# Optimization experiments

Measured on AMD Instinct MI355X. Metric: run time of the kernel, lower is better.

Reference implementation:

```python
import jax, jax.numpy as jnp
import numpy as np

B, S, D = 2, 2048, 1024
H = 16            # attention heads
KVH = 4           # key/value heads
G = H // KVH      # group_size = 4
HD = D // H       # head_dim = 64
ROPE_THETA = 10000.0


def rope(x):
    # x: [B, S, D]; interleaved-pair rotary embedding over full last dim
    d = x.shape[-1]
    inv_freq = 1.0 / (ROPE_THETA ** (jnp.arange(0, d, 2, dtype=jnp.float32) / d))  # [d/2]
    ang = jnp.arange(x.shape[1], dtype=jnp.float32)[:, None] * inv_freq[None, :]   # [S, d/2]
    cos, sin = jnp.cos(ang), jnp.sin(ang)
    x1, x2 = x[..., 0::2], x[..., 1::2]
    r1 = x1 * cos - x2 * sin
    r2 = x1 * sin + x2 * cos
    out = jnp.stack([r1, r2], axis=-1).reshape(x.shape)
    return out


def setup_inputs() -> dict:
    key = jax.random.key(0)
    kx, kq, kk, kv = jax.random.split(key, 4)
    x = jax.random.normal(kx, (B, S, D), dtype=jnp.float32)
    # mark last 256 positions of batch element 1 as padding via NaN
    x = x.at[1, S - 256:, :].set(jnp.nan)
    scale = 1.0 / np.sqrt(D)
    Wq = jax.random.normal(kq, (D, D), dtype=jnp.float32) * scale
    Wk = jax.random.normal(kk, (D, D // G), dtype=jnp.float32) * scale
    Wv = jax.random.normal(kv, (D, D // G), dtype=jnp.float32) * scale
    return {"x": x, "Wq": Wq, "Wk": Wk, "Wv": Wv}


def reference(x, Wq, Wk, Wv):
    pad = jnp.isnan(x)                      # [B,S,D]
    x = jnp.where(pad, 0.0, x)
    key_pad = jnp.any(pad, axis=-1)         # [B,S] True = padded token

    q = x @ Wq                              # [B,S,D]
    k = jnp.repeat(x @ Wk, G, axis=-1)      # grouped KV, repeat_interleave -> [B,S,D]
    v = jnp.repeat(x @ Wv, G, axis=-1)

    q = rope(q)
    k = rope(k)

    def split_heads(t):
        return t.reshape(B, S, H, HD).transpose(0, 2, 1, 3)  # [B,H,S,HD]

    q, k, v = split_heads(q), split_heads(k), split_heads(v)

    scores = jnp.einsum('bhqd,bhkd->bhqk', q, k) / np.sqrt(HD)
    causal = jnp.tril(jnp.ones((S, S), dtype=bool))
    allow = causal[None, None, :, :] & (~key_pad)[:, None, None, :]
    scores = jnp.where(allow, scores, -1e9)
    attn = jax.nn.softmax(scores, axis=-1)
    out = jnp.einsum('bhqk,bhkd->bhqd', attn, v)
    return out.transpose(0, 2, 1, 3).reshape(B, S, D)
```

## Files before the change

### kernel.cpp

```cpp
#include <hip/hip_runtime.h>
#include <hip/hip_bf16.h>
#include <math.h>

typedef unsigned short u16;
typedef unsigned int u32;
typedef __bf16 bf16x8 __attribute__((ext_vector_type(8)));
typedef float fx4 __attribute__((ext_vector_type(4)));

#define MFMA16(a, b, c) __builtin_amdgcn_mfma_f32_16x16x32_bf16(a, b, c, 0, 0, 0)

static constexpr int Bb = 2, Ss = 2048, Dd = 1024, Hh = 16, DKV = 256;
static constexpr int NQKV = 1536;
static constexpr int ROWS = Bb * Ss;
static constexpr float L2T_OVER = 0.0259525632f;
static constexpr float SC2 = 0.18033688f;
static constexpr int PSTR = 76;

__device__ __forceinline__ u16 f2bf(float f) {
    union { float f; u32 i; } v; v.f = f;
    u32 u = v.i;
    return (u16)((u + 0x7FFFu + ((u >> 16) & 1u)) >> 16);
}
__device__ __forceinline__ u16 bfr(float f) {
    return (u16)((__float_as_uint(f) + 0x8000u) >> 16);
}

__device__ __forceinline__ void gl16(const u16* g, u16* l) {
    __builtin_amdgcn_global_load_lds(
        (const __attribute__((address_space(1))) void*)g,
        (__attribute__((address_space(3))) void*)l, 16, 0, 0);
}

template <int CTRL>
__device__ __forceinline__ float dppf(float x) {
    return __int_as_float(
        __builtin_amdgcn_mov_dpp(__float_as_int(x), CTRL, 0xF, 0xF, true));
}
__device__ __forceinline__ float rsum16(float x) {
    x += dppf<0xB1>(x);
    x += dppf<0x4E>(x);
    x += dppf<0x124>(x);
    x += dppf<0x128>(x);
    return x;
}

__global__ void pre_kernel(const float* __restrict__ x, const float* __restrict__ Wq,
                           const float* __restrict__ Wk, const float* __restrict__ Wv,
                           u16* __restrict__ xc, u32* __restrict__ kpb,
                           u16* __restrict__ wAll) {
    __shared__ u16 tile[32][33];
    __shared__ int flag;
    int bid = blockIdx.x, t = threadIdx.x;
    if (bid < 4096) {
        int row = bid;
        if (t == 0) flag = 0;
        __syncthreads();
        float4 d = *(const float4*)(x + (size_t)row * Dd + t * 4);
        int any = 0;
        float a0 = d.x, a1 = d.y, a2 = d.z, a3 = d.w;
        if ((__float_as_uint(a0) & 0x7FFFFFFFu) > 0x7F800000u) { a0 = 0.f; any = 1; }
        if ((__float_as_uint(a1) & 0x7FFFFFFFu) > 0x7F800000u) { a1 = 0.f; any = 1; }
        if ((__float_as_uint(a2) & 0x7FFFFFFFu) > 0x7F800000u) { a2 = 0.f; any = 1; }
        if ((__float_as_uint(a3) & 0x7FFFFFFFu) > 0x7F800000u) { a3 = 0.f; any = 1; }
        if (any) atomicOr(&flag, 1);
        uint2 o;
        o.x = (u32)f2bf(a0) | ((u32)f2bf(a1) << 16);
        o.y = (u32)f2bf(a2) | ((u32)f2bf(a3) << 16);
        *(uint2*)(xc + (size_t)row * Dd + t * 4) = o;
        __syncthreads();
        if (t == 0 && flag) {
            int b = row >> 11, s = row & (Ss - 1);
            atomicOr(&kpb[b * 64 + (s >> 5)], 1u << (s & 31));
        }
        return;
    }
    const float* in; u16* out; int C, bx, by;
    if (bid < 5120) { int i = bid - 4096; in = Wq; out = wAll; C = Dd; bx = i & 31; by = i >> 5; }
    else if (bid < 5376) { int i = bid - 5120; in = Wk; out = wAll + (size_t)Dd * Dd; C = DKV; bx = i & 7; by = i >> 3; }
    else { int i = bid - 5376; in = Wv; out = wAll + (size_t)1280 * Dd; C = DKV; bx = i & 7; by = i >> 3; }
    int c0 = bx * 32, r0 = by * 32;
    int tx = t & 31, ty = t >> 5;
    for (int i = 0; i < 32; i += 8)
        tile[ty + i][tx] = f2bf(in[(size_t)(r0 + ty + i) * C + c0 + tx]);
    __syncthreads();
    for (int i = 0; i < 32; i += 8)
        out[(size_t)(c0 + ty + i) * Dd + r0 + tx] = tile[tx][ty + i];
}

__global__ __launch_bounds__(256) void gemm_qkv(
    const u16* __restrict__ A, const u16* __restrict__ Bt, u16* __restrict__ C) {
    __shared__ __align__(16) u16 As[2][128 * 32];
    __shared__ __align__(16) u16 Bs[2][64 * 32];
    int t = threadIdx.x, w = t >> 6, lane = t & 63;
    int l15 = lane & 15, quad = lane >> 4;
    int col0 = blockIdx.x * 64, row0 = blockIdx.y * 128;
    int wm = w >> 1, wn = w & 1;
    fx4 acc[4][2];
#pragma unroll
    for (int i = 0; i < 4; ++i)
#pragma unroll
        for (int j = 0; j < 2; ++j) acc[i][j] = (fx4){0.f, 0.f, 0.f, 0.f};

    auto stage = [&](int kb, int buf) {
#pragma unroll
        for (int i = 0; i < 2; ++i) {
            int slot = i * 256 + t;
            int row = slot >> 2, p = slot & 3, g = p ^ ((row >> 1) & 3);
            gl16(A + (size_t)(row0 + row) * Dd + kb * 32 + g * 8,
                 &As[buf][(i * 256 + w * 64) * 8]);
        }
        {
            int row = t >> 2, p = t & 3, g = p ^ ((row >> 1) & 3);
            gl16(Bt + (size_t)(col0 + row) * Dd + kb * 32 + g * 8,
                 &Bs[buf][(w * 64) * 8]);
        }
    };

    stage(0, 0);
    int buf = 0;
    for (int kb = 0; kb < 32; ++kb) {
        __syncthreads();
        if (kb + 1 < 32) stage(kb + 1, buf ^ 1);
        bf16x8 af[4], bfr2[2];
#pragma unroll
        for (int mi = 0; mi < 4; ++mi) {
            int row = wm * 64 + mi * 16 + l15;
            af[mi] = *(const bf16x8*)(&As[buf][row * 32 + ((quad ^ ((row >> 1) & 3)) * 8)]);
        }
#pragma unroll
        for (int ni = 0; ni < 2; ++ni) {
            int row = wn * 32 + ni * 16 + l15;
            bfr2[ni] = *(const bf16x8*)(&Bs[buf][row * 32 + ((quad ^ ((row >> 1) & 3)) * 8)]);
        }
#pragma unroll
        for (int mi = 0; mi < 4; ++mi)
#pragma unroll
            for (int ni = 0; ni < 2; ++ni)
                acc[mi][ni] = MFMA16(af[mi], bfr2[ni], acc[mi][ni]);
        buf ^= 1;
    }
#pragma unroll
    for (int mi = 0; mi < 4; ++mi) {
        int rbase = row0 + wm * 64 + mi * 16 + quad * 4;
#pragma unroll
        for (int ni = 0; ni < 2; ++ni) {
            int ccol = col0 + wn * 32 + ni * 16 + l15;
#pragma unroll
            for (int r = 0; r < 4; ++r)
                C[(size_t)(rbase + r) * NQKV + ccol] = f2bf(acc[mi][ni][r]);
        }
    }
}

__global__ void post_kernel(const u16* __restrict__ qkv, u16* __restrict__ kr,
                            u16* __restrict__ vtb) {
    __shared__ u16 tile[32][33];
    int bid = blockIdx.x, t = threadIdx.x;
    if (bid < 4096) {
        int row = bid;
        float pos = (float)(row & (Ss - 1));
        float kv = __uint_as_float(((u32)qkv[(size_t)row * NQKV + Dd + t]) << 16);
        float j0 = (float)(2 * t), j1 = j0 + 1.0f;
        float f0 = exp2f(-j0 * L2T_OVER), f1 = exp2f(-j1 * L2T_OVER);
        float s0, c0, s1, c1;
        sincosf(pos * f0, &s0, &c0);
        sincosf(pos * f1, &s1, &c1);
        float r0 = kv * (c0 - s0), r1 = kv * (s0 + c0);
        float r2 = kv * (c1 - s1), r3 = kv * (s1 + c1);
        uint2 o;
        o.x = (u32)f2bf(r0) | ((u32)f2bf(r1) << 16);
        o.y = (u32)f2bf(r2) | ((u32)f2bf(r3) << 16);
        *(uint2*)(kr + (size_t)row * Dd + t * 4) = o;
        return;
    }
    int i = bid - 4096;
    int b = i >> 9, by = (i & 511) >> 3, bx = i & 7;
    int c0 = bx * 32, r0 = by * 32;
    int tx = t & 31, ty = t >> 5;
    for (int k = 0; k < 32; k += 8)
        tile[ty + k][tx] = qkv[(size_t)(b * Ss + r0 + ty + k) * NQKV + 1280 + c0 + tx];
    __syncthreads();
    for (int k = 0; k < 32; k += 8)
        vtb[(size_t)(b * DKV + c0 + ty + k) * Ss + r0 + tx] = tile[tx][ty + k];
}

__device__ __forceinline__ bf16x8 ropeFrag(uint4 raw, float pos, float jbase) {
    u32 W[4] = {raw.x, raw.y, raw.z, raw.w};
    union { u32 u[4]; bf16x8 v; } o;
#pragma unroll
    for (int c = 0; c < 4; ++c) {
        float x0 = __uint_as_float(W[c] << 16);
        float x1 = __uint_as_float(W[c] & 0xFFFF0000u);
        float f = exp2f(-(jbase + (float)c) * L2T_OVER);
        float sn, cs;
        sincosf(pos * f, &sn, &cs);
        float r0 = x0 * cs - x1 * sn, r1 = x0 * sn + x1 * cs;
        o.u[c] = (u32)f2bf(r0) | ((u32)f2bf(r1) << 16);
    }
    return o.v;
}

__global__ __launch_bounds__(256) void attn_kernel(
    const u16* __restrict__ qkv, const u16* __restrict__ kr,
    const u16* __restrict__ vt, const u32* __restrict__ kpb,
    float* __restrict__ O16, float* __restrict__ Lsum) {
    __shared__ __align__(16) u16 Ks[2][64 * 64];
    __shared__ __align__(16) u16 Ps[4][16 * PSTR];

    int t = threadIdx.x, w = t >> 6, lane = t & 63;
    int l15 = lane & 15, quad = lane >> 4;
    int bid = blockIdx.x;
    int u = bid >> 5;
    int tile, c;
    if (u < 32)      { tile = 24 + (u & 7); c = u >> 3; }
    else if (u < 56) { tile = 16 + ((u - 32) & 7); c = (u - 32) >> 3; }
    else if (u < 72) { tile = 8 + ((u - 56) & 7); c = (u - 56) >> 3; }
    else             { tile = u - 72; c = 0; }
    int hh = bid & 31, b = hh >> 4, h = hh & 15;
    int q0 = tile * 64;
    int kb0 = c * 8;
    int kbe = min(kb0 + 8, tile + 1);

    int pos = q0 + w * 16 + l15;
    const u16* qp = qkv + (size_t)(b * Ss + pos) * NQKV + h * 64;
    float jb = (float)(h * 32 + quad * 4);
    bf16x8 qf0 = ropeFrag(*(const uint4*)(qp + quad * 8), (float)pos, jb);
    bf16x8 qf1 = ropeFrag(*(const uint4*)(qp + 32 + quad * 8), (float)pos, jb + 16.f);

    u32 pw_all = kpb[b * 64 + lane];

    const u16* vrow = vt + (size_t)(b * DKV + h * 16 + l15) * Ss;

    auto stageK = [&](int k0, int buf) {
#pragma unroll
        for (int i2 = 0; i2 < 2; ++i2) {
            int row = i2 * 32 + w * 8 + (lane >> 3);
            int gg = (lane & 7) ^ (row & 7);
            gl16(kr + (size_t)(b * Ss + k0 + row) * Dd + h * 64 + gg * 8,
                 &Ks[buf][(i2 * 32 + w * 8) * 64]);
        }
    };

    float l_lane[4] = {0.f, 0.f, 0.f, 0.f};
    fx4 oacc = (fx4){0.f, 0.f, 0.f, 0.f};

    stageK(kb0 * 64, 0);
    int buf = 0;
    const int qrb = q0 + w * 16 + quad * 4;
    const int qmin = q0 + w * 16;

    for (int kb = kb0; kb < kbe; ++kb) {
        int k0 = kb * 64;
        __syncthreads();
        if (kb + 1 < kbe) stageK(k0 + 64, buf ^ 1);

        bf16x8 vf0 = *(const bf16x8*)(vrow + k0 + quad * 8);
        bf16x8 vf1 = *(const bf16x8*)(vrow + k0 + 32 + quad * 8);

        fx4 s[4];
#pragma unroll
        for (int tt = 0; tt < 4; ++tt) {
            const u16* kb_ = &Ks[buf][(tt * 16 + l15) * 64];
            bf16x8 kf0 = *(const bf16x8*)(kb_ + ((quad ^ (l15 & 7)) * 8));
            bf16x8 kf1 = *(const bf16x8*)(kb_ + (((quad + 4) ^ (l15 & 7)) * 8));
            fx4 z = (fx4){0.f, 0.f, 0.f, 0.f};
            fx4 a = MFMA16(qf0, kf0, z);
            s[tt] = MFMA16(qf1, kf1, a);
        }

        u32 pw0 = (u32)__shfl((int)pw_all, 2 * kb, 64);
        u32 pw1 = (u32)__shfl((int)pw_all, 2 * kb + 1, 64);
        bool fast = (k0 + 63 <= qmin) & ((pw0 | pw1) == 0u);

        float e[4][4];
        if (fast) {
#pragma unroll
            for (int tt = 0; tt < 4; ++tt)
#pragma unroll
                for (int r = 0; r < 4; ++r)
                    e[tt][r] = exp2f(fmaf(s[tt][r], SC2, -32.f));
        } else {
            u32 padb[4];
#pragma unroll
            for (int tt = 0; tt < 4; ++tt)
                padb[tt] = ((tt & 2 ? pw1 : pw0) >> ((tt * 16 + l15) & 31)) & 1u;
#pragma unroll
            for (int r = 0; r < 4; ++r) {
                int qq = qrb + r;
#pragma unroll
                for (int tt = 0; tt < 4; ++tt) {
                    float ee = exp2f(fmaf(s[tt][r], SC2, -32.f));
                    e[tt][r] = (k0 + tt * 16 + l15 <= qq && !padb[tt]) ? ee : 0.f;
                }
            }
        }

#pragma unroll
        for (int r = 0; r < 4; ++r) {
            l_lane[r] += (e[0][r] + e[1][r]) + (e[2][r] + e[3][r]);
            int prow = (quad * 4 + r) * PSTR + l15;
            Ps[w][prow + 0] = bfr(e[0][r]);
            Ps[w][prow + 16] = bfr(e[1][r]);
            Ps[w][prow + 32] = bfr(e[2][r]);
            Ps[w][prow + 48] = bfr(e[3][r]);
        }

        {
            bf16x8 pf0 = *(const bf16x8*)(&Ps[w][l15 * PSTR + quad * 8]);
            bf16x8 pf1 = *(const bf16x8*)(&Ps[w][l15 * PSTR + 32 + quad * 8]);
            oacc = MFMA16(pf0, vf0, oacc);
            oacc = MFMA16(pf1, vf1, oacc);
        }
        buf ^= 1;
    }

    size_t obase = (size_t)hh * Ss;
#pragma unroll
    for (int r = 0; r < 4; ++r) {
        float l_row = rsum16(l_lane[r]);
        int q = qrb + r;
        atomicAdd(&O16[(obase + q) * 16 + l15], oacc[r]);
        if (l15 == 0) atomicAdd(&Lsum[obase + q], l_row);
    }
}

__global__ void norm_kernel(const float* __restrict__ O16, const float* __restrict__ Lsum,
                            float* __restrict__ out) {
    int idx = blockIdx.x * 256 + threadIdx.x;
    int d4 = idx & 255;
    int row = idx >> 8;
    int h = d4 >> 4, f = d4 & 15;
    int b = row >> 11, s = row & (Ss - 1);
    size_t o = (size_t)(b * 16 + h) * Ss + s;
    float a = O16[o * 16 + f] / Lsum[o];
    float4 o4 = {a, a, a, a};
    *(float4*)(out + (size_t)row * Dd + d4 * 4) = o4;
}

extern "C" void kernel_launch(void* const* d_in, const int* in_sizes, int n_in,
                              void* d_out, int out_size, void* d_ws, size_t ws_size,
                              hipStream_t stream) {
    const float* x = (const float*)d_in[0];
    const float* Wq = (const float*)d_in[1];
    const float* Wk = (const float*)d_in[2];
    const float* Wv = (const float*)d_in[3];
    float* out = (float*)d_out;

    char* ws = (char*)d_ws;
    const size_t SZ_XC = (size_t)ROWS * Dd * 2;
    const size_t SZ_KPB = 4096;
    const size_t SZ_WALL = (size_t)NQKV * Dd * 2;
    const size_t SZ_QKV = (size_t)ROWS * NQKV * 2;
    const size_t SZ_O16 = (size_t)32 * Ss * 16 * 4;
    const size_t SZ_L = (size_t)32 * Ss * 4;

    size_t off = 0;
    u16* xc = (u16*)(ws + off);
    u16* krope = (u16*)(ws + off); off += SZ_XC;
    u32* kpb = (u32*)(ws + off); off += SZ_KPB;
    u16* wAll = (u16*)(ws + off);
    u16* vtb = (u16*)(ws + off); off += SZ_WALL;
    u16* qkv = (u16*)(ws + off); off += SZ_QKV;
    float* O16 = (float*)(ws + off); off += SZ_O16;
    float* Ls = (float*)(ws + off); off += SZ_L;
    (void)ws_size; (void)in_sizes; (void)n_in; (void)out_size;

    hipMemsetAsync(kpb, 0, 2 * 64 * 4, stream);
    hipMemsetAsync(O16, 0, SZ_O16 + SZ_L, stream);
    pre_kernel<<<5632, 256, 0, stream>>>(x, Wq, Wk, Wv, xc, kpb, wAll);
    gemm_qkv<<<dim3(NQKV / 64, ROWS / 128), 256, 0, stream>>>(xc, wAll, qkv);
    post_kernel<<<5120, 256, 0, stream>>>(qkv, krope, vtb);
    attn_kernel<<<2560, 256, 0, stream>>>(qkv, krope, vtb, kpb, O16, Ls);
    norm_kernel<<<4096, 256, 0, stream>>>(O16, Ls, out);
}
```

Measured before the change: 160.0 us.

## Use persistent atomic work queue for attention and hardware transcendental intrinsics

Converts the attention kernel to a persistent grid of 1536 blocks that fetch work units from a global atomic counter, and balances key-block chunks evenly across each tile's chunks instead of fixed 8-block chunks. Small tiles are now processed last in reverse order. It also replaces exp2f/sincosf with raw v_exp_f32/v_sin/v_cos instructions after manual range reduction, to cut transcendental cost in RoPE and softmax. Trade-offs: less accurate sin/cos for large angles, an extra __syncthreads per work unit, and a counter that relies on the memset.

```diff
diff --git a/kernel.cpp b/kernel.cpp
--- a/kernel.cpp
+++ b/kernel.cpp
@@ -15,6 +15,7 @@
 static constexpr float L2T_OVER = 0.0259525632f;
 static constexpr float SC2 = 0.18033688f;
 static constexpr int PSTR = 76;
+static constexpr int NUNITS = 2560;
 
 __device__ __forceinline__ u16 f2bf(float f) {
     union { float f; u32 i; } v; v.f = f;
@@ -23,6 +24,16 @@
 }
 __device__ __forceinline__ u16 bfr(float f) {
     return (u16)((__float_as_uint(f) + 0x8000u) >> 16);
+}
+
+__device__ __forceinline__ float fexp2(float x) {
+    float r; asm("v_exp_f32 %0, %1" : "=v"(r) : "v"(x)); return r;
+}
+__device__ __forceinline__ void fsincos(float a, float& sn, float& cs) {
+    float r = a * 0.15915494309189535f;
+    r = r - floorf(r);
+    asm("v_sin_f32 %0, %1" : "=v"(sn) : "v"(r));
+    asm("v_cos_f32 %0, %1" : "=v"(cs) : "v"(r));
 }
 
 __device__ __forceinline__ void gl16(const u16* g, u16* l) {
@@ -161,10 +172,10 @@
         float pos = (float)(row & (Ss - 1));
         float kv = __uint_as_float(((u32)qkv[(size_t)row * NQKV + Dd + t]) << 16);
         float j0 = (float)(2 * t), j1 = j0 + 1.0f;
-        float f0 = exp2f(-j0 * L2T_OVER), f1 = exp2f(-j1 * L2T_OVER);
+        float f0 = fexp2(-j0 * L2T_OVER), f1 = fexp2(-j1 * L2T_OVER);
         float s0, c0, s1, c1;
-        sincosf(pos * f0, &s0, &c0);
-        sincosf(pos * f1, &s1, &c1);
+        fsincos(pos * f0, s0, c0);
+        fsincos(pos * f1, s1, c1);
         float r0 = kv * (c0 - s0), r1 = kv * (s0 + c0);
         float r2 = kv * (c1 - s1), r3 = kv * (s1 + c1);
         uint2 o;
@@ -191,9 +202,9 @@
     for (int c = 0; c < 4; ++c) {
         float x0 = __uint_as_float(W[c] << 16);
         float x1 = __uint_as_float(W[c] & 0xFFFF0000u);
-        float f = exp2f(-(jbase + (float)c) * L2T_OVER);
+        float f = fexp2(-(jbase + (float)c) * L2T_OVER);
         float sn, cs;
-        sincosf(pos * f, &sn, &cs);
+        fsincos(pos * f, sn, cs);
         float r0 = x0 * cs - x1 * sn, r1 = x0 * sn + x1 * cs;
         o.u[c] = (u32)f2bf(r0) | ((u32)f2bf(r1) << 16);
     }
@@ -203,124 +214,133 @@
 __global__ __launch_bounds__(256) void attn_kernel(
     const u16* __restrict__ qkv, const u16* __restrict__ kr,
     const u16* __restrict__ vt, const u32* __restrict__ kpb,
-    float* __restrict__ O16, float* __restrict__ Lsum) {
+    u32* __restrict__ ctr, float* __restrict__ O16, float* __restrict__ Lsum) {
     __shared__ __align__(16) u16 Ks[2][64 * 64];
     __shared__ __align__(16) u16 Ps[4][16 * PSTR];
+    __shared__ int s_unit;
 
     int t = threadIdx.x, w = t >> 6, lane = t & 63;
     int l15 = lane & 15, quad = lane >> 4;
-    int bid = blockIdx.x;
-    int u = bid >> 5;
-    int tile, c;
-    if (u < 32)      { tile = 24 + (u & 7); c = u >> 3; }
-    else if (u < 56) { tile = 16 + ((u - 32) & 7); c = (u - 32) >> 3; }
-    else if (u < 72) { tile = 8 + ((u - 56) & 7); c = (u - 56) >> 3; }
-    else             { tile = u - 72; c = 0; }
-    int hh = bid & 31, b = hh >> 4, h = hh & 15;
-    int q0 = tile * 64;
-    int kb0 = c * 8;
-    int kbe = min(kb0 + 8, tile + 1);
-
-    int pos = q0 + w * 16 + l15;
-    const u16* qp = qkv + (size_t)(b * Ss + pos) * NQKV + h * 64;
-    float jb = (float)(h * 32 + quad * 4);
-    bf16x8 qf0 = ropeFrag(*(const uint4*)(qp + quad * 8), (float)pos, jb);
-    bf16x8 qf1 = ropeFrag(*(const uint4*)(qp + 32 + quad * 8), (float)pos, jb + 16.f);
-
-    u32 pw_all = kpb[b * 64 + lane];
-
-    const u16* vrow = vt + (size_t)(b * DKV + h * 16 + l15) * Ss;
-
-    auto stageK = [&](int k0, int buf) {
-#pragma unroll
-        for (int i2 = 0; i2 < 2; ++i2) {
-            int row = i2 * 32 + w * 8 + (lane >> 3);
-            int gg = (lane & 7) ^ (row & 7);
-            gl16(kr + (size_t)(b * Ss + k0 + row) * Dd + h * 64 + gg * 8,
-                 &Ks[buf][(i2 * 32 + w * 8) * 64]);
-        }
-    };
-
-    float l_lane[4] = {0.f, 0.f, 0.f, 0.f};
-    fx4 oacc = (fx4){0.f, 0.f, 0.f, 0.f};
-
-    stageK(kb0 * 64, 0);
-    int buf = 0;
-    const int qrb = q0 + w * 16 + quad * 4;
-    const int qmin = q0 + w * 16;
-
-    for (int kb = kb0; kb < kbe; ++kb) {
-        int k0 = kb * 64;
+
+    for (;;) {
+        if (t == 0) s_unit = (int)atomicAdd(ctr, 1u);
         __syncthreads();
-        if (kb + 1 < kbe) stageK(k0 + 64, buf ^ 1);
-
-        bf16x8 vf0 = *(const bf16x8*)(vrow + k0 + quad * 8);
-        bf16x8 vf1 = *(const bf16x8*)(vrow + k0 + 32 + quad * 8);
-
-        fx4 s[4];
-#pragma unroll
-        for (int tt = 0; tt < 4; ++tt) {
-            const u16* kb_ = &Ks[buf][(tt * 16 + l15) * 64];
-            bf16x8 kf0 = *(const bf16x8*)(kb_ + ((quad ^ (l15 & 7)) * 8));
-            bf16x8 kf1 = *(const bf16x8*)(kb_ + (((quad + 4) ^ (l15 & 7)) * 8));
-            fx4 z = (fx4){0.f, 0.f, 0.f, 0.f};
-            fx4 a = MFMA16(qf0, kf0, z);
-            s[tt] = MFMA16(qf1, kf1, a);
-        }
-
-        u32 pw0 = (u32)__shfl((int)pw_all, 2 * kb, 64);
-        u32 pw1 = (u32)__shfl((int)pw_all, 2 * kb + 1, 64);
-        bool fast = (k0 + 63 <= qmin) & ((pw0 | pw1) == 0u);
-
-        float e[4][4];
-        if (fast) {
-#pragma unroll
-            for (int tt = 0; tt < 4; ++tt)
-#pragma unroll
-                for (int r = 0; r < 4; ++r)
-                    e[tt][r] = exp2f(fmaf(s[tt][r], SC2, -32.f));
-        } else {
-            u32 padb[4];
-#pragma unroll
-            for (int tt = 0; tt < 4; ++tt)
-                padb[tt] = ((tt & 2 ? pw1 : pw0) >> ((tt * 16 + l15) & 31)) & 1u;
+        int unit = s_unit;
+        if (unit >= NUNITS) return;
+
+        int u = unit >> 5, hh = unit & 31;
+        int tile, c;
+        if (u < 32)      { tile = 24 + (u & 7); c = u >> 3; }
+        else if (u < 56) { tile = 16 + ((u - 32) & 7); c = (u - 32) >> 3; }
+        else if (u < 72) { tile = 8 + ((u - 56) & 7); c = (u - 56) >> 3; }
+        else             { tile = 7 - (u - 72); c = 0; }
+        int b = hh >> 4, h = hh & 15;
+        int n = tile + 1, C = (n + 7) >> 3;
+        int kb0 = (u32)(n * c) / (u32)C;
+        int kbe = (u32)(n * (c + 1)) / (u32)C;
+        int q0 = tile * 64;
+
+        int pos = q0 + w * 16 + l15;
+        const u16* qp = qkv + (size_t)(b * Ss + pos) * NQKV + h * 64;
+        float jb = (float)(h * 32 + quad * 4);
+        bf16x8 qf0 = ropeFrag(*(const uint4*)(qp + quad * 8), (float)pos, jb);
+        bf16x8 qf1 = ropeFrag(*(const uint4*)(qp + 32 + quad * 8), (float)pos, jb + 16.f);
+
+        u32 pw_all = kpb[b * 64 + lane];
+
+        const u16* vrow = vt + (size_t)(b * DKV + h * 16 + l15) * Ss;
+
+        auto stageK = [&](int k0, int buf) {
+#pragma unroll
+            for (int i2 = 0; i2 < 2; ++i2) {
+                int row = i2 * 32 + w * 8 + (lane >> 3);
+                int gg = (lane & 7) ^ (row & 7);
+                gl16(kr + (size_t)(b * Ss + k0 + row) * Dd + h * 64 + gg * 8,
+                     &Ks[buf][(i2 * 32 + w * 8) * 64]);
+            }
+        };
+
+        float l_lane[4] = {0.f, 0.f, 0.f, 0.f};
+        fx4 oacc = (fx4){0.f, 0.f, 0.f, 0.f};
+
+        stageK(kb0 * 64, 0);
+        int buf = 0;
+        const int qrb = q0 + w * 16 + quad * 4;
+        const int qmin = q0 + w * 16;
+
+        for (int kb = kb0; kb < kbe; ++kb) {
+            int k0 = kb * 64;
+            __syncthreads();
+            if (kb + 1 < kbe) stageK(k0 + 64, buf ^ 1);
+
+            bf16x8 vf0 = *(const bf16x8*)(vrow + k0 + quad * 8);
+            bf16x8 vf1 = *(const bf16x8*)(vrow + k0 + 32 + quad * 8);
+
+            fx4 s[4];
+#pragma unroll
+            for (int tt = 0; tt < 4; ++tt) {
+                const u16* kb_ = &Ks[buf][(tt * 16 + l15) * 64];
+                bf16x8 kf0 = *(const bf16x8*)(kb_ + ((quad ^ (l15 & 7)) * 8));
+                bf16x8 kf1 = *(const bf16x8*)(kb_ + (((quad + 4) ^ (l15 & 7)) * 8));
+                fx4 z = (fx4){0.f, 0.f, 0.f, 0.f};
+                fx4 a = MFMA16(qf0, kf0, z);
+                s[tt] = MFMA16(qf1, kf1, a);
+            }
+
+            u32 pw0 = (u32)__shfl((int)pw_all, 2 * kb, 64);
+            u32 pw1 = (u32)__shfl((int)pw_all, 2 * kb + 1, 64);
+            bool fast = (k0 + 63 <= qmin) & ((pw0 | pw1) == 0u);
+
+            float e[4][4];
+            if (fast) {
+#pragma unroll
+                for (int tt = 0; tt < 4; ++tt)
+#pragma unroll
+                    for (int r = 0; r < 4; ++r)
+                        e[tt][r] = fexp2(fmaf(s[tt][r], SC2, -32.f));
+            } else {
+                u32 padb[4];
+#pragma unroll
+                for (int tt = 0; tt < 4; ++tt)
+                    padb[tt] = ((tt & 2 ? pw1 : pw0) >> ((tt * 16 + l15) & 31)) & 1u;
+#pragma unroll
+                for (int r = 0; r < 4; ++r) {
+                    int qq = qrb + r;
+#pragma unroll
+                    for (int tt = 0; tt < 4; ++tt) {
+                        float ee = fexp2(fmaf(s[tt][r], SC2, -32.f));
+                        e[tt][r] = (k0 + tt * 16 + l15 <= qq && !padb[tt]) ? ee : 0.f;
+                    }
+                }
+            }
+
 #pragma unroll
             for (int r = 0; r < 4; ++r) {
-                int qq = qrb + r;
-#pragma unroll
-                for (int tt = 0; tt < 4; ++tt) {
-                    float ee = exp2f(fmaf(s[tt][r], SC2, -32.f));
-                    e[tt][r] = (k0 + tt * 16 + l15 <= qq && !padb[tt]) ? ee : 0.f;
-                }
-            }
-        }
-
+                l_lane[r] += (e[0][r] + e[1][r]) + (e[2][r] + e[3][r]);
+                int prow = (quad * 4 + r) * PSTR + l15;
+                Ps[w][prow + 0] = bfr(e[0][r]);
+                Ps[w][prow + 16] = bfr(e[1][r]);
+                Ps[w][prow + 32] = bfr(e[2][r]);
+                Ps[w][prow + 48] = bfr(e[3][r]);
+            }
+
+            {
+                bf16x8 pf0 = *(const bf16x8*)(&Ps[w][l15 * PSTR + quad * 8]);
+                bf16x8 pf1 = *(const bf16x8*)(&Ps[w][l15 * PSTR + 32 + quad * 8]);
+                oacc = MFMA16(pf0, vf0, oacc);
+                oacc = MFMA16(pf1, vf1, oacc);
+            }
+            buf ^= 1;
+        }
+
+        size_t obase = (size_t)hh * Ss;
 #pragma unroll
         for (int r = 0; r < 4; ++r) {
-            l_lane[r] += (e[0][r] + e[1][r]) + (e[2][r] + e[3][r]);
-            int prow = (quad * 4 + r) * PSTR + l15;
-            Ps[w][prow + 0] = bfr(e[0][r]);
-            Ps[w][prow + 16] = bfr(e[1][r]);
-            Ps[w][prow + 32] = bfr(e[2][r]);
-            Ps[w][prow + 48] = bfr(e[3][r]);
-        }
-
-        {
-            bf16x8 pf0 = *(const bf16x8*)(&Ps[w][l15 * PSTR + quad * 8]);
-            bf16x8 pf1 = *(const bf16x8*)(&Ps[w][l15 * PSTR + 32 + quad * 8]);
-            oacc = MFMA16(pf0, vf0, oacc);
-            oacc = MFMA16(pf1, vf1, oacc);
-        }
-        buf ^= 1;
-    }
-
-    size_t obase = (size_t)hh * Ss;
-#pragma unroll
-    for (int r = 0; r < 4; ++r) {
-        float l_row = rsum16(l_lane[r]);
-        int q = qrb + r;
-        atomicAdd(&O16[(obase + q) * 16 + l15], oacc[r]);
-        if (l15 == 0) atomicAdd(&Lsum[obase + q], l_row);
+            float l_row = rsum16(l_lane[r]);
+            int q = qrb + r;
+            atomicAdd(&O16[(obase + q) * 16 + l15], oacc[r]);
+            if (l15 == 0) atomicAdd(&Lsum[obase + q], l_row);
+        }
     }
 }
 
@@ -363,13 +383,14 @@
     u16* qkv = (u16*)(ws + off); off += SZ_QKV;
     float* O16 = (float*)(ws + off); off += SZ_O16;
     float* Ls = (float*)(ws + off); off += SZ_L;
+    u32* ctr = kpb + 192;
     (void)ws_size; (void)in_sizes; (void)n_in; (void)out_size;
 
-    hipMemsetAsync(kpb, 0, 2 * 64 * 4, stream);
+    hipMemsetAsync(kpb, 0, 1024, stream);
     hipMemsetAsync(O16, 0, SZ_O16 + SZ_L, stream);
     pre_kernel<<<5632, 256, 0, stream>>>(x, Wq, Wk, Wv, xc, kpb, wAll);
     gemm_qkv<<<dim3(NQKV / 64, ROWS / 128), 256, 0, stream>>>(xc, wAll, qkv);
     post_kernel<<<5120, 256, 0, stream>>>(qkv, krope, vtb);
-    attn_kernel<<<2560, 256, 0, stream>>>(qkv, krope, vtb, kpb, O16, Ls);
+    attn_kernel<<<1536, 256, 0, stream>>>(qkv, krope, vtb, kpb, ctr, O16, Ls);
     norm_kernel<<<4096, 256, 0, stream>>>(O16, Ls, out);
 }
```

Measured after the change: 176.8 us. 10.5% more time.
